# Performance work log

Hardware: AMD Instinct MI355X
Metric: run time of the kernel (lower is better)

## Reference

```python
import jax, jax.numpy as jnp
import numpy as np

N_HEADS = 4

def setup_inputs() -> dict:
    key = jax.random.key(0)
    B, S, D = 4, 2048, 256
    ks = jax.random.split(key, 9)
    sd = 1.0 / np.sqrt(D)
    return {
        "x":  jax.random.normal(ks[0], (B, S, D), jnp.float32),
        "Wq": jax.random.normal(ks[1], (D, D), jnp.float32) * sd,
        "bq": jax.random.normal(ks[2], (D,), jnp.float32) * 0.02,
        "Wk": jax.random.normal(ks[3], (D, D), jnp.float32) * sd,
        "bk": jax.random.normal(ks[4], (D,), jnp.float32) * 0.02,
        "Wv": jax.random.normal(ks[5], (D, D), jnp.float32) * sd,
        "bv": jax.random.normal(ks[6], (D,), jnp.float32) * 0.02,
        "Wo": jax.random.normal(ks[7], (D, D), jnp.float32) * sd,
        "bo": jax.random.normal(ks[8], (D,), jnp.float32) * 0.02,
    }

def reference(x, Wq, bq, Wk, bk, Wv, bv, Wo, bo):
    B, S, D = x.shape
    H = N_HEADS
    W = D // H
    # QKV projections, split heads: (B,S,D) -> (B,H,S,W)
    def heads(t):
        return t.reshape(B, S, H, W).transpose(0, 2, 1, 3)
    q = heads(x @ Wq + bq)
    k = heads(x @ Wk + bk)
    v = heads(x @ Wv + bv)
    scores = jnp.einsum('bhqw,bhkw->bhqk', q, k) / jnp.sqrt(jnp.float32(W))
    # multiplicative distance-decay mask: mask[i,j] = (S - |i-j|)/S
    i = jnp.arange(S, dtype=jnp.float32)
    mask = (S - jnp.abs(i[:, None] - i[None, :])) / S  # (S,S)
    scores = jax.nn.softmax(scores * mask, axis=-1)
    h = jnp.einsum('bhqk,bhkw->bhqw', scores, v)
    h = h.transpose(0, 2, 1, 3).reshape(B, S, D)  # merge heads
    return h @ Wo + bo
```

## Files before the change

kernel.cpp:

```cpp
#include <hip/hip_runtime.h>
#include <hip/hip_bf16.h>

#define S_LEN 2048
#define DMODEL 256
#define NH 4
#define HDIM 64

typedef __attribute__((ext_vector_type(8))) short short8;
typedef __attribute__((ext_vector_type(4))) float floatx4;
typedef __hip_bfloat16 bf16;

__device__ __forceinline__ floatx4 mfma16(short8 a, short8 b, floatx4 c) {
    return __builtin_amdgcn_mfma_f32_16x16x32_bf16(a, b, c, 0, 0, 0);
}
__device__ __forceinline__ void gload16(const void* gp, void* lp) {
    __builtin_amdgcn_global_load_lds(
        (const __attribute__((address_space(1))) void*)gp,
        (__attribute__((address_space(3))) void*)lp, 16, 0, 0);
}
__device__ __forceinline__ unsigned cvtpk(float lo, float hi) {
    unsigned r;
    asm("v_cvt_pk_bf16_f32 %0, %1, %2" : "=v"(r) : "v"(lo), "v"(hi));
    return r;
}
__device__ __forceinline__ void p32swap(int &a, int &b) {
    auto res = __builtin_amdgcn_permlane32_swap((unsigned)a, (unsigned)b, false, false);
    a = (int)res[0]; b = (int)res[1];
}

__global__ __launch_bounds__(256) void prep_kernel(
    const float* __restrict__ x,
    const float* __restrict__ Wq, const float* __restrict__ Wk,
    const float* __restrict__ Wv, const float* __restrict__ Wo,
    bf16* __restrict__ xb, bf16* __restrict__ wtq, bf16* __restrict__ wtk,
    bf16* __restrict__ wtv, bf16* __restrict__ wto)
{
    __shared__ bf16 sT[64 * 72];
    const int t = threadIdx.x;
    const int blk = blockIdx.x;
    if (blk < 256) {
        int base = blk * 8192 + t * 8;
#pragma unroll
        for (int j = 0; j < 4; ++j) {
            int idx = base + j * 2048;
            float4 f0 = *(const float4*)&x[idx];
            float4 f1 = *(const float4*)&x[idx + 4];
            union { bf16 h[8]; short8 v; } o;
            o.h[0] = __float2bfloat16(f0.x); o.h[1] = __float2bfloat16(f0.y);
            o.h[2] = __float2bfloat16(f0.z); o.h[3] = __float2bfloat16(f0.w);
            o.h[4] = __float2bfloat16(f1.x); o.h[5] = __float2bfloat16(f1.y);
            o.h[6] = __float2bfloat16(f1.z); o.h[7] = __float2bfloat16(f1.w);
            *(short8*)&xb[idx] = o.v;
        }
    } else {
        int blk2 = blk - 256;
        int wi = blk2 >> 2;
        int n0 = (blk2 & 3) * 64;
        const float* ws = (wi == 0) ? Wq : (wi == 1) ? Wk : (wi == 2) ? Wv : Wo;
        bf16* wd = (wi == 0) ? wtq : (wi == 1) ? wtk : (wi == 2) ? wtv : wto;
        for (int k0 = 0; k0 < 256; k0 += 64) {
            __syncthreads();
#pragma unroll
            for (int j = 0; j < 16; ++j) {
                int idx = j * 256 + t;
                int kk = idx >> 6, nn = idx & 63;
                sT[nn * 72 + kk] = __float2bfloat16(ws[(k0 + kk) * 256 + n0 + nn]);
            }
            __syncthreads();
#pragma unroll
            for (int j2 = 0; j2 < 2; ++j2) {
                int c = j2 * 256 + t;
                int nn = c >> 3, seg = c & 7;
                *(short8*)&wd[(n0 + nn) * 256 + k0 + seg * 8] = *(const short8*)&sT[nn * 72 + seg * 8];
            }
        }
    }
}

__global__ __launch_bounds__(256) void proj_qk_kernel(
    const bf16* __restrict__ xb, const bf16* __restrict__ wtq, const bf16* __restrict__ wtk,
    const float* __restrict__ bq, const float* __restrict__ bk,
    bf16* __restrict__ qo, bf16* __restrict__ ko)
{
    __shared__ __align__(16) char sm[2 * 24576];
    const bf16* wt = blockIdx.z ? wtk : wtq;
    const float* bias = blockIdx.z ? bk : bq;
    bf16* dst = blockIdx.z ? ko : qo;
    const int t = threadIdx.x, wid = t >> 6, lane = t & 63;
    const int g = lane >> 4, r = lane & 15;
    const int m0 = blockIdx.x * 128, n0 = blockIdx.y * 64;
    const int wm = wid >> 1, wn = wid & 1;

    const bf16* srcA[4]; const bf16* srcB[2];
    int ldsA[4], ldsB[2];
#pragma unroll
    for (int j = 0; j < 4; ++j) {
        int c = j * 256 + t;
        int row = c >> 3, seg = c & 7, segx = seg ^ (row & 7);
        srcA[j] = xb + (m0 + row) * 256 + segx * 8;
        ldsA[j] = (j * 256 + wid * 64) * 16;
    }
#pragma unroll
    for (int j = 0; j < 2; ++j) {
        int c = j * 256 + t;
        int row = c >> 3, seg = c & 7, segx = seg ^ (row & 7);
        srcB[j] = wt + (n0 + row) * 256 + segx * 8;
        ldsB[j] = 16384 + (j * 256 + wid * 64) * 16;
    }
    const int xk0 = ((0 + g) ^ (r & 7)) * 8 + r * 64;
    const int xk1 = ((4 + g) ^ (r & 7)) * 8 + r * 64;

    floatx4 acc[4][2];
#pragma unroll
    for (int a = 0; a < 4; ++a)
#pragma unroll
        for (int b2 = 0; b2 < 2; ++b2) acc[a][b2] = (floatx4)0.f;

#pragma unroll
    for (int j = 0; j < 4; ++j) { gload16(srcA[j], sm + ldsA[j]); srcA[j] += 64; }
#pragma unroll
    for (int j = 0; j < 2; ++j) { gload16(srcB[j], sm + ldsB[j]); srcB[j] += 64; }
    __syncthreads();

    for (int kt = 0; kt < 4; ++kt) {
        int buf = kt & 1;
        if (kt < 3) {
            char* nb = sm + (buf ^ 1) * 24576;
#pragma unroll
            for (int j = 0; j < 4; ++j) { gload16(srcA[j], nb + ldsA[j]); srcA[j] += 64; }
#pragma unroll
            for (int j = 0; j < 2; ++j) { gload16(srcB[j], nb + ldsB[j]); srcB[j] += 64; }
        }
        const bf16* A = (const bf16*)(sm + buf * 24576);
        const bf16* B = (const bf16*)(sm + buf * 24576 + 16384);
        short8 af[4][2], bfr[2][2];
#pragma unroll
        for (int mf = 0; mf < 4; ++mf) {
            int rb = (wm * 64 + mf * 16) * 64;
            af[mf][0] = *(const short8*)&A[rb + xk0];
            af[mf][1] = *(const short8*)&A[rb + xk1];
        }
#pragma unroll
        for (int nf = 0; nf < 2; ++nf) {
            int rb = (wn * 32 + nf * 16) * 64;
            bfr[nf][0] = *(const short8*)&B[rb + xk0];
            bfr[nf][1] = *(const short8*)&B[rb + xk1];
        }
#pragma unroll
        for (int kf = 0; kf < 2; ++kf)
#pragma unroll
            for (int mf = 0; mf < 4; ++mf)
#pragma unroll
                for (int nf = 0; nf < 2; ++nf)
                    acc[mf][nf] = mfma16(af[mf][kf], bfr[nf][kf], acc[mf][nf]);
        __syncthreads();
    }
#pragma unroll
    for (int mf = 0; mf < 4; ++mf)
#pragma unroll
        for (int nf = 0; nf < 2; ++nf) {
            int n = n0 + wn * 32 + nf * 16 + r;
            float bv2 = bias[n];
            int h = n >> 6, ww = n & 63;
#pragma unroll
            for (int i = 0; i < 4; ++i) {
                int m = m0 + wm * 64 + mf * 16 + g * 4 + i;
                int b = m >> 11, s = m & 2047;
                dst[(((b * NH + h) * S_LEN) + s) * HDIM + ww] = __float2bfloat16(acc[mf][nf][i] + bv2);
            }
        }
}

__global__ __launch_bounds__(256) void proj_v_kernel(
    const bf16* __restrict__ xb, const bf16* __restrict__ wtv,
    const float* __restrict__ bvb, bf16* __restrict__ vt)
{
    __shared__ __align__(16) char sm[2 * 24576];
    const int t = threadIdx.x, wid = t >> 6, lane = t & 63;
    const int g = lane >> 4, r = lane & 15;
    const int m0 = blockIdx.x * 128, n0 = blockIdx.y * 64;
    const int wm = wid >> 1, wn = wid & 1;

    const bf16* srcB[4]; const bf16* srcA[2];
    int ldsB[4], ldsA[2];
#pragma unroll
    for (int j = 0; j < 4; ++j) {
        int c = j * 256 + t;
        int row = c >> 3, seg = c & 7, segx = seg ^ (row & 7);
        srcB[j] = xb + (m0 + row) * 256 + segx * 8;
        ldsB[j] = (j * 256 + wid * 64) * 16;
    }
#pragma unroll
    for (int j = 0; j < 2; ++j) {
        int c = j * 256 + t;
        int row = c >> 3, seg = c & 7, segx = seg ^ (row & 7);
        srcA[j] = wtv + (n0 + row) * 256 + segx * 8;
        ldsA[j] = 16384 + (j * 256 + wid * 64) * 16;
    }
    const int xk0 = ((0 + g) ^ (r & 7)) * 8 + r * 64;
    const int xk1 = ((4 + g) ^ (r & 7)) * 8 + r * 64;

    floatx4 acc[2][4];
#pragma unroll
    for (int a = 0; a < 2; ++a)
#pragma unroll
        for (int b2 = 0; b2 < 4; ++b2) acc[a][b2] = (floatx4)0.f;

#pragma unroll
    for (int j = 0; j < 4; ++j) { gload16(srcB[j], sm + ldsB[j]); srcB[j] += 64; }
#pragma unroll
    for (int j = 0; j < 2; ++j) { gload16(srcA[j], sm + ldsA[j]); srcA[j] += 64; }
    __syncthreads();

    for (int kt = 0; kt < 4; ++kt) {
        int buf = kt & 1;
        if (kt < 3) {
            char* nb = sm + (buf ^ 1) * 24576;
#pragma unroll
            for (int j = 0; j < 4; ++j) { gload16(srcB[j], nb + ldsB[j]); srcB[j] += 64; }
#pragma unroll
            for (int j = 0; j < 2; ++j) { gload16(srcA[j], nb + ldsA[j]); srcA[j] += 64; }
        }
        const bf16* Bx = (const bf16*)(sm + buf * 24576);
        const bf16* Aw = (const bf16*)(sm + buf * 24576 + 16384);
        short8 af[2][2], bfr[4][2];
#pragma unroll
        for (int mf = 0; mf < 2; ++mf) {
            int rb = (wm * 32 + mf * 16) * 64;
            af[mf][0] = *(const short8*)&Aw[rb + xk0];
            af[mf][1] = *(const short8*)&Aw[rb + xk1];
        }
#pragma unroll
        for (int nf = 0; nf < 4; ++nf) {
            int rb = (wn * 64 + nf * 16) * 64;
            bfr[nf][0] = *(const short8*)&Bx[rb + xk0];
            bfr[nf][1] = *(const short8*)&Bx[rb + xk1];
        }
#pragma unroll
        for (int kf = 0; kf < 2; ++kf)
#pragma unroll
            for (int mf = 0; mf < 2; ++mf)
#pragma unroll
                for (int nf = 0; nf < 4; ++nf)
                    acc[mf][nf] = mfma16(af[mf][kf], bfr[nf][kf], acc[mf][nf]);
        __syncthreads();
    }
#pragma unroll
    for (int mf = 0; mf < 2; ++mf)
#pragma unroll
        for (int nf = 0; nf < 4; ++nf)
#pragma unroll
            for (int i = 0; i < 4; ++i) {
                int feat = n0 + wm * 32 + mf * 16 + g * 4 + i;
                int scol = m0 + wn * 64 + nf * 16 + r;
                float v = acc[mf][nf][i] + bvb[feat];
                int b = scol >> 11, s = scol & 2047;
                vt[((size_t)((b * NH + (feat >> 6)) * HDIM + (feat & 63))) * S_LEN + s] = __float2bfloat16(v);
            }
}

__global__ __launch_bounds__(256) void proj_o_kernel(
    const bf16* __restrict__ hb, const bf16* __restrict__ wto,
    const float* __restrict__ bo, float* __restrict__ out)
{
    __shared__ __align__(16) char sm[2 * 24576];
    const int t = threadIdx.x, wid = t >> 6, lane = t & 63;
    const int g = lane >> 4, r = lane & 15;
    const int m0 = blockIdx.x * 128, n0 = blockIdx.y * 64;
    const int wm = wid >> 1, wn = wid & 1;

    const bf16* srcA[4]; const bf16* srcB[2];
    int ldsA[4], ldsB[2];
#pragma unroll
    for (int j = 0; j < 4; ++j) {
        int c = j * 256 + t;
        int row = c >> 3, seg = c & 7, segx = seg ^ (row & 7);
        srcA[j] = hb + (m0 + row) * 256 + segx * 8;
        ldsA[j] = (j * 256 + wid * 64) * 16;
    }
#pragma unroll
    for (int j = 0; j < 2; ++j) {
        int c = j * 256 + t;
        int row = c >> 3, seg = c & 7, segx = seg ^ (row & 7);
        srcB[j] = wto + (n0 + row) * 256 + segx * 8;
        ldsB[j] = 16384 + (j * 256 + wid * 64) * 16;
    }
    const int xk0 = ((0 + g) ^ (r & 7)) * 8 + r * 64;
    const int xk1 = ((4 + g) ^ (r & 7)) * 8 + r * 64;

    floatx4 acc[4][2];
#pragma unroll
    for (int a = 0; a < 4; ++a)
#pragma unroll
        for (int b2 = 0; b2 < 2; ++b2) acc[a][b2] = (floatx4)0.f;

#pragma unroll
    for (int j = 0; j < 4; ++j) { gload16(srcA[j], sm + ldsA[j]); srcA[j] += 64; }
#pragma unroll
    for (int j = 0; j < 2; ++j) { gload16(srcB[j], sm + ldsB[j]); srcB[j] += 64; }
    __syncthreads();

    for (int kt = 0; kt < 4; ++kt) {
        int buf = kt & 1;
        if (kt < 3) {
            char* nb = sm + (buf ^ 1) * 24576;
#pragma unroll
            for (int j = 0; j < 4; ++j) { gload16(srcA[j], nb + ldsA[j]); srcA[j] += 64; }
#pragma unroll
            for (int j = 0; j < 2; ++j) { gload16(srcB[j], nb + ldsB[j]); srcB[j] += 64; }
        }
        const bf16* A = (const bf16*)(sm + buf * 24576);
        const bf16* B = (const bf16*)(sm + buf * 24576 + 16384);
        short8 af[4][2], bfr[2][2];
#pragma unroll
        for (int mf = 0; mf < 4; ++mf) {
            int rb = (wm * 64 + mf * 16) * 64;
            af[mf][0] = *(const short8*)&A[rb + xk0];
            af[mf][1] = *(const short8*)&A[rb + xk1];
        }
#pragma unroll
        for (int nf = 0; nf < 2; ++nf) {
            int rb = (wn * 32 + nf * 16) * 64;
            bfr[nf][0] = *(const short8*)&B[rb + xk0];
            bfr[nf][1] = *(const short8*)&B[rb + xk1];
        }
#pragma unroll
        for (int kf = 0; kf < 2; ++kf)
#pragma unroll
            for (int mf = 0; mf < 4; ++mf)
#pragma unroll
                for (int nf = 0; nf < 2; ++nf)
                    acc[mf][nf] = mfma16(af[mf][kf], bfr[nf][kf], acc[mf][nf]);
        __syncthreads();
    }
#pragma unroll
    for (int mf = 0; mf < 4; ++mf)
#pragma unroll
        for (int nf = 0; nf < 2; ++nf) {
            int n = n0 + wn * 32 + nf * 16 + r;
            float bv2 = bo[n];
#pragma unroll
            for (int i = 0; i < 4; ++i) {
                int m = m0 + wm * 64 + mf * 16 + g * 4 + i;
                out[(size_t)m * 256 + n] = acc[mf][nf][i] + bv2;
            }
        }
}

__global__ __launch_bounds__(512, 4) void attn_kernel(
    const bf16* __restrict__ q, const bf16* __restrict__ kmat,
    const bf16* __restrict__ vt, bf16* __restrict__ hout)
{
    __shared__ __align__(16) char smem[65536];
    const int t = threadIdx.x, wid = t >> 6, lane = t & 63;
    const int g = lane >> 4, r = lane & 15;
    const int qg = wid >> 1, hh = wid & 1;
    const int F = blockIdx.y * 32 + blockIdx.x;
    const int bh = ((F & 7) << 1) | ((F >> 3) & 1);
    const int q0 = (F >> 4) * 64;

    const bf16* srcp[4]; int ldsoff[4]; int sstride[4];
#pragma unroll
    for (int qi = 0; qi < 4; ++qi) {
        int idx = wid * 4 + qi;
        int arr = idx >> 3;
        int chunkbase = (idx & 7) * 64;
        int chunk = chunkbase + lane;
        int row = chunk >> 3, seg = chunk & 7, segx = seg ^ (row & 7);
        if (arr < 2) {
            srcp[qi] = kmat + ((size_t)(bh * S_LEN + arr * 1024 + row)) * HDIM + segx * 8;
            sstride[qi] = 64 * HDIM;
        } else {
            srcp[qi] = vt + ((size_t)(bh * HDIM + row)) * S_LEN + (arr - 2) * 1024 + segx * 8;
            sstride[qi] = 64;
        }
        ldsoff[qi] = arr * 8192 + chunkbase * 16;
    }

    const bf16* qb = q + ((size_t)(bh * S_LEN + q0 + qg * 16 + r)) * HDIM;
    short8 qf0 = *(const short8*)&qb[g * 8];
    short8 qf1 = *(const short8*)&qb[32 + g * 8];

    const int xk0 = ((0 + g) ^ (r & 7)) * 8 + r * 64;
    const int xk1 = ((4 + g) ^ (r & 7)) * 8 + r * 64;

    floatx4 oacc[4];
#pragma unroll
    for (int nf = 0; nf < 4; ++nf) oacc[nf] = (floatx4)0.f;
    float m_run = -1e30f, l_run = 0.f;

    const float iqf = (float)(q0 + qg * 16 + r);
    const float e0 = iqf - (float)(g * 4);
    const float CN = 6.103515625e-05f;
    const bool godd = (lane & 16) != 0;

#pragma unroll
    for (int qi = 0; qi < 4; ++qi) { gload16(srcp[qi], smem + ldsoff[qi]); srcp[qi] += sstride[qi]; }
    __syncthreads();

    for (int it = 0; it < 16; ++it) {
        int buf = it & 1;
        if (it < 15) {
            char* nb = smem + (buf ^ 1) * 32768;
#pragma unroll
            for (int qi = 0; qi < 4; ++qi) { gload16(srcp[qi], nb + ldsoff[qi]); srcp[qi] += sstride[qi]; }
        }
        const bf16* sK = (const bf16*)(smem + buf * 32768 + hh * 8192);
        const bf16* sV = (const bf16*)(smem + buf * 32768 + 16384 + hh * 8192);

        floatx4 sc[4];
#pragma unroll
        for (int nt = 0; nt < 4; ++nt) sc[nt] = (floatx4)0.f;
#pragma unroll
        for (int nt = 0; nt < 4; ++nt) {
            short8 kf0 = *(const short8*)&sK[nt * 1024 + xk0];
            short8 kf1 = *(const short8*)&sK[nt * 1024 + xk1];
            sc[nt] = mfma16(kf0, qf0, sc[nt]);
            sc[nt] = mfma16(kf1, qf1, sc[nt]);
        }
        int kv0 = hh * 1024 + it * 64;
        float u_ = e0 - (float)kv0;
#pragma unroll
        for (int nt = 0; nt < 4; ++nt) {
            float tnt = u_ - (float)(nt * 16);
#pragma unroll
            for (int i = 0; i < 4; ++i) {
                float d = tnt - (float)i;
                float mmv = fmaf(fabsf(d), -CN, 0.125f);
                sc[nt][i] *= mmv;
            }
        }
        float vm = sc[0][0];
#pragma unroll
        for (int nt = 0; nt < 4; ++nt)
#pragma unroll
            for (int i = 0; i < 4; ++i) vm = fmaxf(vm, sc[nt][i]);
        vm = fmaxf(vm, __shfl_xor(vm, 16));
        vm = fmaxf(vm, __shfl_xor(vm, 32));
        float mn = fmaxf(m_run, vm);
        float c_ = __expf(m_run - mn);
        m_run = mn;
        float s0 = 0.f;
#pragma unroll
        for (int nt = 0; nt < 4; ++nt)
#pragma unroll
            for (int i = 0; i < 4; ++i) {
                float p = __expf(sc[nt][i] - mn);
                sc[nt][i] = p;
                s0 += p;
            }
        s0 += __shfl_xor(s0, 16);
        s0 += __shfl_xor(s0, 32);
        l_run = l_run * c_ + s0;
#pragma unroll
        for (int nf = 0; nf < 4; ++nf)
#pragma unroll
            for (int i = 0; i < 4; ++i) oacc[nf][i] *= c_;

        int wp[4][2];
#pragma unroll
        for (int nt = 0; nt < 4; ++nt) {
            wp[nt][0] = (int)cvtpk(sc[nt][0], sc[nt][1]);
            wp[nt][1] = (int)cvtpk(sc[nt][2], sc[nt][3]);
        }
        short8 pfrag[2];
#pragma unroll
        for (int kf = 0; kf < 2; ++kf) {
            int a0 = wp[2 * kf][0], a1 = wp[2 * kf][1];
            int b0 = wp[2 * kf + 1][0], b1 = wp[2 * kf + 1][1];
            p32swap(a0, b0);
            p32swap(a1, b1);
            int sx0 = __shfl_xor(a0, 16);
            int sy0 = __shfl_xor(b0, 16);
            int sx1 = __shfl_xor(a1, 16);
            int sy1 = __shfl_xor(b1, 16);
            union { int u[4]; short8 s; } pf;
            pf.u[0] = godd ? sy0 : a0;
            pf.u[1] = godd ? sy1 : a1;
            pf.u[2] = godd ? b0 : sx0;
            pf.u[3] = godd ? b1 : sx1;
            pfrag[kf] = pf.s;
        }
#pragma unroll
        for (int nf = 0; nf < 4; ++nf) {
            short8 vf0 = *(const short8*)&sV[nf * 1024 + xk0];
            short8 vf1 = *(const short8*)&sV[nf * 1024 + xk1];
            oacc[nf] = mfma16(vf0, pfrag[0], oacc[nf]);
            oacc[nf] = mfma16(vf1, pfrag[1], oacc[nf]);
        }
        __syncthreads();
    }

    float* sO = (float*)smem;
    float* sml = (float*)(smem + 16896);
    if (hh == 1) {
#pragma unroll
        for (int nf = 0; nf < 4; ++nf)
#pragma unroll
            for (int i = 0; i < 4; ++i)
                sO[(qg * 16 + r) * 66 + nf * 16 + g * 4 + i] = oacc[nf][i];
        if (g == 0) {
            sml[(qg * 16 + r) * 2 + 0] = m_run;
            sml[(qg * 16 + r) * 2 + 1] = l_run;
        }
    }
    __syncthreads();
    if (hh == 0) {
        float pm = sml[(qg * 16 + r) * 2 + 0];
        float pl = sml[(qg * 16 + r) * 2 + 1];
        float M = fmaxf(m_run, pm);
        float c0 = __expf(m_run - M), c1 = __expf(pm - M);
        float rec = 1.f / (c0 * l_run + c1 * pl);
        int b = bh >> 2, hd = bh & 3;
        int srow = q0 + qg * 16 + r;
        bf16* outp = hout + ((size_t)(b * S_LEN + srow)) * DMODEL + hd * HDIM;
#pragma unroll
        for (int nf = 0; nf < 4; ++nf) {
            union { bf16 h[4]; unsigned long long u; } ov;
#pragma unroll
            for (int i = 0; i < 4; ++i) {
                float po = sO[(qg * 16 + r) * 66 + nf * 16 + g * 4 + i];
                ov.h[i] = __float2bfloat16((c0 * oacc[nf][i] + c1 * po) * rec);
            }
            *(unsigned long long*)&outp[nf * 16 + g * 4] = ov.u;
        }
    }
}

extern "C" void kernel_launch(void* const* d_in, const int* in_sizes, int n_in,
                              void* d_out, int out_size, void* d_ws, size_t ws_size,
                              hipStream_t stream) {
    const float* x  = (const float*)d_in[0];
    const float* Wq = (const float*)d_in[1];
    const float* bq = (const float*)d_in[2];
    const float* Wk = (const float*)d_in[3];
    const float* bk = (const float*)d_in[4];
    const float* Wv = (const float*)d_in[5];
    const float* bv = (const float*)d_in[6];
    const float* Wo = (const float*)d_in[7];
    const float* bo = (const float*)d_in[8];

    char* ws = (char*)d_ws;
    bf16* xb  = (bf16*)(ws + 0);
    bf16* wtq = (bf16*)(ws + 4194304);
    bf16* wtk = (bf16*)(ws + 4325376);
    bf16* wtv = (bf16*)(ws + 4456448);
    bf16* wto = (bf16*)(ws + 4587520);
    bf16* qws = (bf16*)(ws + 4718592);
    bf16* kws = (bf16*)(ws + 8912896);
    bf16* vtw = (bf16*)(ws + 13107200);
    bf16* hws = (bf16*)(ws + 17301504);

    prep_kernel<<<272, 256, 0, stream>>>(x, Wq, Wk, Wv, Wo, xb, wtq, wtk, wtv, wto);
    proj_qk_kernel<<<dim3(64, 4, 2), 256, 0, stream>>>(xb, wtq, wtk, bq, bk, qws, kws);
    proj_v_kernel<<<dim3(64, 4), 256, 0, stream>>>(xb, wtv, bv, vtw);
    attn_kernel<<<dim3(32, 16), 512, 0, stream>>>(qws, kws, vtw, hws);
    proj_o_kernel<<<dim3(64, 4), 256, 0, stream>>>(hws, wto, bo, (float*)d_out);
}
```

Measured before the change: 135.7 us.

## Unify projection GEMMs into one kernel, lazy softmax rescale, exp2 and permlane16

The three projection kernels become a single mode-switched kernel with 64x64 tiles that load the full K=256 into LDS at once. Q, K and V now run in one launch, and the output projection reuses the same kernel. In attention, the scale is folded into log2e so exp2 can be used, and the running max is only updated when a tile exceeds it by more than a threshold, which skips the rescale of oacc. The P-fragment shuffles are replaced with permlane16_swap, and s_setprio is placed around the MFMA blocks. The lazy rescale keeps results correct because the row sum is rescaled consistently, but it allows exponents up to 2^8, which costs some bf16 precision headroom.

New measurement: 129.5 us. 4.5% less time.

```diff
diff --git a/kernel.cpp b/kernel.cpp
--- a/kernel.cpp
+++ b/kernel.cpp
@@ -26,6 +26,22 @@
 __device__ __forceinline__ void p32swap(int &a, int &b) {
     auto res = __builtin_amdgcn_permlane32_swap((unsigned)a, (unsigned)b, false, false);
     a = (int)res[0]; b = (int)res[1];
+}
+#if __has_builtin(__builtin_amdgcn_permlane16_swap)
+#define HAVE_P16 1
+__device__ __forceinline__ void p16swap(int &a, int &b) {
+    auto res = __builtin_amdgcn_permlane16_swap((unsigned)a, (unsigned)b, false, false);
+    a = (int)res[0]; b = (int)res[1];
+}
+#else
+#define HAVE_P16 0
+#endif
+__device__ __forceinline__ float ex2(float x) {
+#if __has_builtin(__builtin_amdgcn_exp2f)
+    return __builtin_amdgcn_exp2f(x);
+#else
+    return __expf(x * 0.6931471805599453f);
+#endif
 }
 
 __global__ __launch_bounds__(256) void prep_kernel(
@@ -77,274 +93,102 @@
     }
 }
 
-__global__ __launch_bounds__(256) void proj_qk_kernel(
-    const bf16* __restrict__ xb, const bf16* __restrict__ wtq, const bf16* __restrict__ wtk,
+__global__ __launch_bounds__(256) void proj_kernel(
+    const bf16* __restrict__ xb, const bf16* __restrict__ hb,
+    const bf16* __restrict__ wtq, const bf16* __restrict__ wtk,
+    const bf16* __restrict__ wtv, const bf16* __restrict__ wto,
     const float* __restrict__ bq, const float* __restrict__ bk,
-    bf16* __restrict__ qo, bf16* __restrict__ ko)
+    const float* __restrict__ bvb, const float* __restrict__ bo,
+    bf16* __restrict__ qo, bf16* __restrict__ ko, bf16* __restrict__ vt,
+    float* __restrict__ oout, int mode_base)
 {
-    __shared__ __align__(16) char sm[2 * 24576];
-    const bf16* wt = blockIdx.z ? wtk : wtq;
-    const float* bias = blockIdx.z ? bk : bq;
-    bf16* dst = blockIdx.z ? ko : qo;
-    const int t = threadIdx.x, wid = t >> 6, lane = t & 63;
+    __shared__ __align__(16) char sm[65536];
+    const int t = threadIdx.x, w = t >> 6, lane = t & 63;
     const int g = lane >> 4, r = lane & 15;
-    const int m0 = blockIdx.x * 128, n0 = blockIdx.y * 64;
-    const int wm = wid >> 1, wn = wid & 1;
-
-    const bf16* srcA[4]; const bf16* srcB[2];
-    int ldsA[4], ldsB[2];
-#pragma unroll
-    for (int j = 0; j < 4; ++j) {
-        int c = j * 256 + t;
-        int row = c >> 3, seg = c & 7, segx = seg ^ (row & 7);
-        srcA[j] = xb + (m0 + row) * 256 + segx * 8;
-        ldsA[j] = (j * 256 + wid * 64) * 16;
-    }
-#pragma unroll
-    for (int j = 0; j < 2; ++j) {
-        int c = j * 256 + t;
-        int row = c >> 3, seg = c & 7, segx = seg ^ (row & 7);
-        srcB[j] = wt + (n0 + row) * 256 + segx * 8;
-        ldsB[j] = 16384 + (j * 256 + wid * 64) * 16;
-    }
-    const int xk0 = ((0 + g) ^ (r & 7)) * 8 + r * 64;
-    const int xk1 = ((4 + g) ^ (r & 7)) * 8 + r * 64;
-
-    floatx4 acc[4][2];
-#pragma unroll
-    for (int a = 0; a < 4; ++a)
-#pragma unroll
-        for (int b2 = 0; b2 < 2; ++b2) acc[a][b2] = (floatx4)0.f;
-
-#pragma unroll
-    for (int j = 0; j < 4; ++j) { gload16(srcA[j], sm + ldsA[j]); srcA[j] += 64; }
-#pragma unroll
-    for (int j = 0; j < 2; ++j) { gload16(srcB[j], sm + ldsB[j]); srcB[j] += 64; }
+    const int mode = mode_base + blockIdx.z;
+    const int bx = blockIdx.x, by = blockIdx.y;
+
+    const char* Asrc; const char* Bsrc;
+    if (mode == 0)      { Asrc = (const char*)(xb  + (size_t)bx * 64 * 256); Bsrc = (const char*)(wtq + (size_t)by * 64 * 256); }
+    else if (mode == 1) { Asrc = (const char*)(xb  + (size_t)bx * 64 * 256); Bsrc = (const char*)(wtk + (size_t)by * 64 * 256); }
+    else if (mode == 2) { Asrc = (const char*)(wtv + (size_t)by * 64 * 256); Bsrc = (const char*)(xb  + (size_t)bx * 64 * 256); }
+    else                { Asrc = (const char*)(hb  + (size_t)bx * 64 * 256); Bsrc = (const char*)(wto + (size_t)by * 64 * 256); }
+
+    const int row8 = t >> 5;
+    const int w16 = t & 31;
+#pragma unroll
+    for (int c = 0; c < 8; ++c) {
+        int row = c * 8 + row8;
+        int sw = w16 ^ (row & 15);
+        gload16(Asrc + row * 512 + sw * 16, sm + row * 512 + w16 * 16);
+    }
+#pragma unroll
+    for (int c = 0; c < 8; ++c) {
+        int row = c * 8 + row8;
+        int sw = w16 ^ (row & 15);
+        gload16(Bsrc + row * 512 + sw * 16, sm + 32768 + row * 512 + w16 * 16);
+    }
     __syncthreads();
 
-    for (int kt = 0; kt < 4; ++kt) {
-        int buf = kt & 1;
-        if (kt < 3) {
-            char* nb = sm + (buf ^ 1) * 24576;
-#pragma unroll
-            for (int j = 0; j < 4; ++j) { gload16(srcA[j], nb + ldsA[j]); srcA[j] += 64; }
-#pragma unroll
-            for (int j = 0; j < 2; ++j) { gload16(srcB[j], nb + ldsB[j]); srcB[j] += 64; }
-        }
-        const bf16* A = (const bf16*)(sm + buf * 24576);
-        const bf16* B = (const bf16*)(sm + buf * 24576 + 16384);
-        short8 af[4][2], bfr[2][2];
-#pragma unroll
-        for (int mf = 0; mf < 4; ++mf) {
-            int rb = (wm * 64 + mf * 16) * 64;
-            af[mf][0] = *(const short8*)&A[rb + xk0];
-            af[mf][1] = *(const short8*)&A[rb + xk1];
-        }
-#pragma unroll
-        for (int nf = 0; nf < 2; ++nf) {
-            int rb = (wn * 32 + nf * 16) * 64;
-            bfr[nf][0] = *(const short8*)&B[rb + xk0];
-            bfr[nf][1] = *(const short8*)&B[rb + xk1];
-        }
-#pragma unroll
-        for (int kf = 0; kf < 2; ++kf)
-#pragma unroll
-            for (int mf = 0; mf < 4; ++mf)
-#pragma unroll
-                for (int nf = 0; nf < 2; ++nf)
-                    acc[mf][nf] = mfma16(af[mf][kf], bfr[nf][kf], acc[mf][nf]);
-        __syncthreads();
-    }
-#pragma unroll
-    for (int mf = 0; mf < 4; ++mf)
-#pragma unroll
-        for (int nf = 0; nf < 2; ++nf) {
-            int n = n0 + wn * 32 + nf * 16 + r;
-            float bv2 = bias[n];
+    const bf16* A = (const bf16*)sm;
+    const bf16* B = (const bf16*)(sm + 32768);
+
+    short8 af[8];
+#pragma unroll
+    for (int kf = 0; kf < 8; ++kf)
+        af[kf] = *(const short8*)&A[(w * 16 + r) * 256 + (((kf * 4 + g) ^ r) * 8)];
+
+    floatx4 acc[4];
+#pragma unroll
+    for (int nf = 0; nf < 4; ++nf) acc[nf] = (floatx4)0.f;
+#pragma unroll
+    for (int kf = 0; kf < 8; ++kf) {
+#pragma unroll
+        for (int nf = 0; nf < 4; ++nf) {
+            short8 bfr = *(const short8*)&B[(nf * 16 + r) * 256 + (((kf * 4 + g) ^ r) * 8)];
+            acc[nf] = mfma16(af[kf], bfr, acc[nf]);
+        }
+    }
+
+    if (mode <= 1) {
+        const float* bias = mode ? bk : bq;
+        bf16* dst = mode ? ko : qo;
+#pragma unroll
+        for (int nf = 0; nf < 4; ++nf) {
+            int n = by * 64 + nf * 16 + r;
+            float bb = bias[n];
             int h = n >> 6, ww = n & 63;
 #pragma unroll
             for (int i = 0; i < 4; ++i) {
-                int m = m0 + wm * 64 + mf * 16 + g * 4 + i;
+                int m = bx * 64 + w * 16 + g * 4 + i;
                 int b = m >> 11, s = m & 2047;
-                dst[(((b * NH + h) * S_LEN) + s) * HDIM + ww] = __float2bfloat16(acc[mf][nf][i] + bv2);
-            }
-        }
-}
-
-__global__ __launch_bounds__(256) void proj_v_kernel(
-    const bf16* __restrict__ xb, const bf16* __restrict__ wtv,
-    const float* __restrict__ bvb, bf16* __restrict__ vt)
-{
-    __shared__ __align__(16) char sm[2 * 24576];
-    const int t = threadIdx.x, wid = t >> 6, lane = t & 63;
-    const int g = lane >> 4, r = lane & 15;
-    const int m0 = blockIdx.x * 128, n0 = blockIdx.y * 64;
-    const int wm = wid >> 1, wn = wid & 1;
-
-    const bf16* srcB[4]; const bf16* srcA[2];
-    int ldsB[4], ldsA[2];
-#pragma unroll
-    for (int j = 0; j < 4; ++j) {
-        int c = j * 256 + t;
-        int row = c >> 3, seg = c & 7, segx = seg ^ (row & 7);
-        srcB[j] = xb + (m0 + row) * 256 + segx * 8;
-        ldsB[j] = (j * 256 + wid * 64) * 16;
-    }
-#pragma unroll
-    for (int j = 0; j < 2; ++j) {
-        int c = j * 256 + t;
-        int row = c >> 3, seg = c & 7, segx = seg ^ (row & 7);
-        srcA[j] = wtv + (n0 + row) * 256 + segx * 8;
-        ldsA[j] = 16384 + (j * 256 + wid * 64) * 16;
-    }
-    const int xk0 = ((0 + g) ^ (r & 7)) * 8 + r * 64;
-    const int xk1 = ((4 + g) ^ (r & 7)) * 8 + r * 64;
-
-    floatx4 acc[2][4];
-#pragma unroll
-    for (int a = 0; a < 2; ++a)
-#pragma unroll
-        for (int b2 = 0; b2 < 4; ++b2) acc[a][b2] = (floatx4)0.f;
-
-#pragma unroll
-    for (int j = 0; j < 4; ++j) { gload16(srcB[j], sm + ldsB[j]); srcB[j] += 64; }
-#pragma unroll
-    for (int j = 0; j < 2; ++j) { gload16(srcA[j], sm + ldsA[j]); srcA[j] += 64; }
-    __syncthreads();
-
-    for (int kt = 0; kt < 4; ++kt) {
-        int buf = kt & 1;
-        if (kt < 3) {
-            char* nb = sm + (buf ^ 1) * 24576;
-#pragma unroll
-            for (int j = 0; j < 4; ++j) { gload16(srcB[j], nb + ldsB[j]); srcB[j] += 64; }
-#pragma unroll
-            for (int j = 0; j < 2; ++j) { gload16(srcA[j], nb + ldsA[j]); srcA[j] += 64; }
-        }
-        const bf16* Bx = (const bf16*)(sm + buf * 24576);
-        const bf16* Aw = (const bf16*)(sm + buf * 24576 + 16384);
-        short8 af[2][2], bfr[4][2];
-#pragma unroll
-        for (int mf = 0; mf < 2; ++mf) {
-            int rb = (wm * 32 + mf * 16) * 64;
-            af[mf][0] = *(const short8*)&Aw[rb + xk0];
-            af[mf][1] = *(const short8*)&Aw[rb + xk1];
-        }
-#pragma unroll
-        for (int nf = 0; nf < 4; ++nf) {
-            int rb = (wn * 64 + nf * 16) * 64;
-            bfr[nf][0] = *(const short8*)&Bx[rb + xk0];
-            bfr[nf][1] = *(const short8*)&Bx[rb + xk1];
-        }
-#pragma unroll
-        for (int kf = 0; kf < 2; ++kf)
-#pragma unroll
-            for (int mf = 0; mf < 2; ++mf)
-#pragma unroll
-                for (int nf = 0; nf < 4; ++nf)
-                    acc[mf][nf] = mfma16(af[mf][kf], bfr[nf][kf], acc[mf][nf]);
-        __syncthreads();
-    }
-#pragma unroll
-    for (int mf = 0; mf < 2; ++mf)
-#pragma unroll
-        for (int nf = 0; nf < 4; ++nf)
-#pragma unroll
-            for (int i = 0; i < 4; ++i) {
-                int feat = n0 + wm * 32 + mf * 16 + g * 4 + i;
-                int scol = m0 + wn * 64 + nf * 16 + r;
-                float v = acc[mf][nf][i] + bvb[feat];
+                dst[(((b * NH + h) * S_LEN) + s) * HDIM + ww] = __float2bfloat16(acc[nf][i] + bb);
+            }
+        }
+    } else if (mode == 2) {
+#pragma unroll
+        for (int sf = 0; sf < 4; ++sf) {
+#pragma unroll
+            for (int i = 0; i < 4; ++i) {
+                int feat = by * 64 + w * 16 + g * 4 + i;
+                int scol = bx * 64 + sf * 16 + r;
+                float v = acc[sf][i] + bvb[feat];
                 int b = scol >> 11, s = scol & 2047;
                 vt[((size_t)((b * NH + (feat >> 6)) * HDIM + (feat & 63))) * S_LEN + s] = __float2bfloat16(v);
             }
-}
-
-__global__ __launch_bounds__(256) void proj_o_kernel(
-    const bf16* __restrict__ hb, const bf16* __restrict__ wto,
-    const float* __restrict__ bo, float* __restrict__ out)
-{
-    __shared__ __align__(16) char sm[2 * 24576];
-    const int t = threadIdx.x, wid = t >> 6, lane = t & 63;
-    const int g = lane >> 4, r = lane & 15;
-    const int m0 = blockIdx.x * 128, n0 = blockIdx.y * 64;
-    const int wm = wid >> 1, wn = wid & 1;
-
-    const bf16* srcA[4]; const bf16* srcB[2];
-    int ldsA[4], ldsB[2];
-#pragma unroll
-    for (int j = 0; j < 4; ++j) {
-        int c = j * 256 + t;
-        int row = c >> 3, seg = c & 7, segx = seg ^ (row & 7);
-        srcA[j] = hb + (m0 + row) * 256 + segx * 8;
-        ldsA[j] = (j * 256 + wid * 64) * 16;
-    }
-#pragma unroll
-    for (int j = 0; j < 2; ++j) {
-        int c = j * 256 + t;
-        int row = c >> 3, seg = c & 7, segx = seg ^ (row & 7);
-        srcB[j] = wto + (n0 + row) * 256 + segx * 8;
-        ldsB[j] = 16384 + (j * 256 + wid * 64) * 16;
-    }
-    const int xk0 = ((0 + g) ^ (r & 7)) * 8 + r * 64;
-    const int xk1 = ((4 + g) ^ (r & 7)) * 8 + r * 64;
-
-    floatx4 acc[4][2];
-#pragma unroll
-    for (int a = 0; a < 4; ++a)
-#pragma unroll
-        for (int b2 = 0; b2 < 2; ++b2) acc[a][b2] = (floatx4)0.f;
-
-#pragma unroll
-    for (int j = 0; j < 4; ++j) { gload16(srcA[j], sm + ldsA[j]); srcA[j] += 64; }
-#pragma unroll
-    for (int j = 0; j < 2; ++j) { gload16(srcB[j], sm + ldsB[j]); srcB[j] += 64; }
-    __syncthreads();
-
-    for (int kt = 0; kt < 4; ++kt) {
-        int buf = kt & 1;
-        if (kt < 3) {
-            char* nb = sm + (buf ^ 1) * 24576;
-#pragma unroll
-            for (int j = 0; j < 4; ++j) { gload16(srcA[j], nb + ldsA[j]); srcA[j] += 64; }
-#pragma unroll
-            for (int j = 0; j < 2; ++j) { gload16(srcB[j], nb + ldsB[j]); srcB[j] += 64; }
-        }
-        const bf16* A = (const bf16*)(sm + buf * 24576);
-        const bf16* B = (const bf16*)(sm + buf * 24576 + 16384);
-        short8 af[4][2], bfr[2][2];
-#pragma unroll
-        for (int mf = 0; mf < 4; ++mf) {
-            int rb = (wm * 64 + mf * 16) * 64;
-            af[mf][0] = *(const short8*)&A[rb + xk0];
-            af[mf][1] = *(const short8*)&A[rb + xk1];
-        }
-#pragma unroll
-        for (int nf = 0; nf < 2; ++nf) {
-            int rb = (wn * 32 + nf * 16) * 64;
-            bfr[nf][0] = *(const short8*)&B[rb + xk0];
-            bfr[nf][1] = *(const short8*)&B[rb + xk1];
-        }
-#pragma unroll
-        for (int kf = 0; kf < 2; ++kf)
-#pragma unroll
-            for (int mf = 0; mf < 4; ++mf)
-#pragma unroll
-                for (int nf = 0; nf < 2; ++nf)
-                    acc[mf][nf] = mfma16(af[mf][kf], bfr[nf][kf], acc[mf][nf]);
-        __syncthreads();
-    }
-#pragma unroll
-    for (int mf = 0; mf < 4; ++mf)
-#pragma unroll
-        for (int nf = 0; nf < 2; ++nf) {
-            int n = n0 + wn * 32 + nf * 16 + r;
-            float bv2 = bo[n];
-#pragma unroll
-            for (int i = 0; i < 4; ++i) {
-                int m = m0 + wm * 64 + mf * 16 + g * 4 + i;
-                out[(size_t)m * 256 + n] = acc[mf][nf][i] + bv2;
-            }
-        }
+        }
+    } else {
+#pragma unroll
+        for (int nf = 0; nf < 4; ++nf) {
+            int n = by * 64 + nf * 16 + r;
+            float bb = bo[n];
+#pragma unroll
+            for (int i = 0; i < 4; ++i) {
+                int m = bx * 64 + w * 16 + g * 4 + i;
+                oout[(size_t)m * 256 + n] = acc[nf][i] + bb;
+            }
+        }
+    }
 }
 
 __global__ __launch_bounds__(512, 4) void attn_kernel(
@@ -391,8 +235,8 @@
 
     const float iqf = (float)(q0 + qg * 16 + r);
     const float e0 = iqf - (float)(g * 4);
-    const float CN = 6.103515625e-05f;
-    const bool godd = (lane & 16) != 0;
+    const float C2  = 0.125f * 1.4426950408889634f;
+    const float CN2 = 1.4426950408889634f / 16384.0f;
 
 #pragma unroll
     for (int qi = 0; qi < 4; ++qi) { gload16(srcp[qi], smem + ldsoff[qi]); srcp[qi] += sstride[qi]; }
@@ -411,6 +255,7 @@
         floatx4 sc[4];
 #pragma unroll
         for (int nt = 0; nt < 4; ++nt) sc[nt] = (floatx4)0.f;
+        __builtin_amdgcn_s_setprio(1);
 #pragma unroll
         for (int nt = 0; nt < 4; ++nt) {
             short8 kf0 = *(const short8*)&sK[nt * 1024 + xk0];
@@ -418,6 +263,7 @@
             sc[nt] = mfma16(kf0, qf0, sc[nt]);
             sc[nt] = mfma16(kf1, qf1, sc[nt]);
         }
+        __builtin_amdgcn_s_setprio(0);
         int kv0 = hh * 1024 + it * 64;
         float u_ = e0 - (float)kv0;
 #pragma unroll
@@ -426,7 +272,7 @@
 #pragma unroll
             for (int i = 0; i < 4; ++i) {
                 float d = tnt - (float)i;
-                float mmv = fmaf(fabsf(d), -CN, 0.125f);
+                float mmv = fmaf(fabsf(d), -CN2, C2);
                 sc[nt][i] *= mmv;
             }
         }
@@ -437,25 +283,28 @@
             for (int i = 0; i < 4; ++i) vm = fmaxf(vm, sc[nt][i]);
         vm = fmaxf(vm, __shfl_xor(vm, 16));
         vm = fmaxf(vm, __shfl_xor(vm, 32));
-        float mn = fmaxf(m_run, vm);
-        float c_ = __expf(m_run - mn);
-        m_run = mn;
+        if (!__all(vm <= m_run + 8.0f)) {
+            float mn = fmaxf(m_run, vm);
+            float c_ = ex2(m_run - mn);
+            m_run = mn;
+            l_run *= c_;
+#pragma unroll
+            for (int nf = 0; nf < 4; ++nf)
+#pragma unroll
+                for (int i = 0; i < 4; ++i) oacc[nf][i] *= c_;
+        }
         float s0 = 0.f;
 #pragma unroll
         for (int nt = 0; nt < 4; ++nt)
 #pragma unroll
             for (int i = 0; i < 4; ++i) {
-                float p = __expf(sc[nt][i] - mn);
+                float p = ex2(sc[nt][i] - m_run);
                 sc[nt][i] = p;
                 s0 += p;
             }
         s0 += __shfl_xor(s0, 16);
         s0 += __shfl_xor(s0, 32);
-        l_run = l_run * c_ + s0;
-#pragma unroll
-        for (int nf = 0; nf < 4; ++nf)
-#pragma unroll
-            for (int i = 0; i < 4; ++i) oacc[nf][i] *= c_;
+        l_run += s0;
 
         int wp[4][2];
 #pragma unroll
@@ -470,17 +319,25 @@
             int b0 = wp[2 * kf + 1][0], b1 = wp[2 * kf + 1][1];
             p32swap(a0, b0);
             p32swap(a1, b1);
+            union { int u[4]; short8 s; } pf;
+#if HAVE_P16
+            p16swap(a0, b0);
+            p16swap(a1, b1);
+            pf.u[0] = a0; pf.u[1] = a1; pf.u[2] = b0; pf.u[3] = b1;
+#else
+            const bool godd = (lane & 16) != 0;
             int sx0 = __shfl_xor(a0, 16);
             int sy0 = __shfl_xor(b0, 16);
             int sx1 = __shfl_xor(a1, 16);
             int sy1 = __shfl_xor(b1, 16);
-            union { int u[4]; short8 s; } pf;
             pf.u[0] = godd ? sy0 : a0;
             pf.u[1] = godd ? sy1 : a1;
             pf.u[2] = godd ? b0 : sx0;
             pf.u[3] = godd ? b1 : sx1;
+#endif
             pfrag[kf] = pf.s;
         }
+        __builtin_amdgcn_s_setprio(1);
 #pragma unroll
         for (int nf = 0; nf < 4; ++nf) {
             short8 vf0 = *(const short8*)&sV[nf * 1024 + xk0];
@@ -488,6 +345,7 @@
             oacc[nf] = mfma16(vf0, pfrag[0], oacc[nf]);
             oacc[nf] = mfma16(vf1, pfrag[1], oacc[nf]);
         }
+        __builtin_amdgcn_s_setprio(0);
         __syncthreads();
     }
 
@@ -509,7 +367,7 @@
         float pm = sml[(qg * 16 + r) * 2 + 0];
         float pl = sml[(qg * 16 + r) * 2 + 1];
         float M = fmaxf(m_run, pm);
-        float c0 = __expf(m_run - M), c1 = __expf(pm - M);
+        float c0 = ex2(m_run - M), c1 = ex2(pm - M);
         float rec = 1.f / (c0 * l_run + c1 * pl);
         int b = bh >> 2, hd = bh & 3;
         int srow = q0 + qg * 16 + r;
@@ -552,8 +410,11 @@
     bf16* hws = (bf16*)(ws + 17301504);
 
     prep_kernel<<<272, 256, 0, stream>>>(x, Wq, Wk, Wv, Wo, xb, wtq, wtk, wtv, wto);
-    proj_qk_kernel<<<dim3(64, 4, 2), 256, 0, stream>>>(xb, wtq, wtk, bq, bk, qws, kws);
-    proj_v_kernel<<<dim3(64, 4), 256, 0, stream>>>(xb, wtv, bv, vtw);
+    proj_kernel<<<dim3(128, 4, 3), 256, 0, stream>>>(xb, hws, wtq, wtk, wtv, wto,
+                                                     bq, bk, bv, bo, qws, kws, vtw,
+                                                     (float*)d_out, 0);
     attn_kernel<<<dim3(32, 16), 512, 0, stream>>>(qws, kws, vtw, hws);
-    proj_o_kernel<<<dim3(64, 4), 256, 0, stream>>>(hws, wto, bo, (float*)d_out);
-}
+    proj_kernel<<<dim3(128, 4, 1), 256, 0, stream>>>(xb, hws, wtq, wtk, wtv, wto,
+                                                     bq, bk, bv, bo, qws, kws, vtw,
+                                                     (float*)d_out, 3);
+}
```
